# Optimization experiments

Measured on AMD Instinct MI355X. Metric: run time of the kernel, lower is better.

## Reference

```python
import jax, jax.numpy as jnp
import numpy as np


def _gcn_conv(x, edge_index, W, b):
    # PyG GCNConv: linear transform, add self-loops, symmetric deg^{-1/2} norm,
    # scatter-add aggregation from source (row) into target (col), then bias.
    N = x.shape[0]
    h = x @ W  # [N, out]
    loops = jnp.arange(N, dtype=edge_index.dtype)
    row = jnp.concatenate([edge_index[0], loops])  # sources j
    col = jnp.concatenate([edge_index[1], loops])  # targets i
    deg = jax.ops.segment_sum(jnp.ones_like(col, dtype=h.dtype), col, num_segments=N)
    dinv = jnp.where(deg > 0, jax.lax.rsqrt(deg), 0.0)
    norm = dinv[row] * dinv[col]  # [E+N]
    msgs = norm[:, None] * h[row]  # gather + scale
    out = jax.ops.segment_sum(msgs, col, num_segments=N)  # scatter-add
    return out + b


def setup_inputs() -> dict:
    key = jax.random.key(0)
    k1, k2, k3, k4 = jax.random.split(key, 4)
    N, E, F, H = 100000, 3200000, 128, 64
    x = jax.random.normal(k1, (N, F), dtype=jnp.float32)
    edge_index = jax.random.randint(k2, (2, E), 0, N, dtype=jnp.int64)
    W1 = jax.random.normal(k3, (F, H), dtype=jnp.float32) * (1.0 / np.sqrt(F))
    b1 = jnp.zeros((H,), dtype=jnp.float32)
    W2 = jax.random.normal(k4, (H, 1), dtype=jnp.float32) * (1.0 / np.sqrt(H))
    b2 = jnp.zeros((1,), dtype=jnp.float32)
    return {"x": x, "edge_index": edge_index, "W1": W1, "b1": b1, "W2": W2, "b2": b2}


def reference(x, edge_index, W1, b1, W2, b2):
    # eval mode: dropout is identity
    h = _gcn_conv(x, edge_index, W1, b1)
    h = jax.nn.relu(h)
    h = _gcn_conv(h, edge_index, W2, b2)  # [N, 1]
    return jnp.mean(h, axis=0)  # [1]
```

## Files before the change

kernel.cpp:

```cpp
#include <hip/hip_runtime.h>
#include <hip/hip_bf16.h>
#include <stdint.h>


#define F_IN 128
#define H_DIM 64
#define BKT_SH 7
#define BKT_SZ 128
#define MAXBKT 1024
#define PWG 256
#define PTHR 256
#define FINBLK 2048

typedef int   i4 __attribute__((ext_vector_type(4)));
typedef float f4 __attribute__((ext_vector_type(4)));
typedef float fv2 __attribute__((ext_vector_type(2)));

#if defined(__has_builtin)
#if __has_builtin(__builtin_amdgcn_cvt_pk_f32_fp8) && __has_builtin(__builtin_amdgcn_cvt_pk_fp8_f32)
#define HW_FP8 1
#endif
#endif

__device__ __forceinline__ float sw_dec_e4m3(unsigned b) {
    unsigned s = b & 0x80, e = (b >> 3) & 15, mm = b & 7;
    float v;
    if (e) v = __uint_as_float(((e + 120u) << 23) | (mm << 20));
    else   v = (float)mm * 0.001953125f;
    return s ? -v : v;
}
__device__ __forceinline__ unsigned sw_enc_e4m3(float f) {
    unsigned s = (__float_as_uint(f) & 0x80000000u) ? 0x80u : 0u;
    float a = fminf(fabsf(f), 448.0f);
    if (a < 9.765625e-4f) return s;
    if (a < 0.015625f) {
        int k = (int)rintf(a * 512.0f);
        if (k > 7) return s | 0x08;
        return s | (unsigned)k;
    }
    int e; float mant = frexpf(a, &e);
    int q = (int)rintf((mant * 2.0f - 1.0f) * 8.0f);
    int E = e - 1;
    if (q == 8) { q = 0; E += 1; }
    if (E > 8) { E = 8; q = 6; }
    return s | ((unsigned)(E + 7) << 3) | (unsigned)q;
}

__device__ __forceinline__ float2 f8pair(unsigned u) {
#ifdef HW_FP8
    fv2 r = __builtin_amdgcn_cvt_pk_f32_fp8((int)u, false);
    return make_float2(r.x, r.y);
#else
    return make_float2(sw_dec_e4m3(u & 0xff), sw_dec_e4m3((u >> 8) & 0xff));
#endif
}
__device__ __forceinline__ unsigned f8pack4(float v0, float v1, float v2, float v3) {
#ifdef HW_FP8
    unsigned pk = (unsigned)__builtin_amdgcn_cvt_pk_fp8_f32(v0, v1, 0, false);
    pk = (unsigned)__builtin_amdgcn_cvt_pk_fp8_f32(v2, v3, (int)pk, true);
    return pk;
#else
    return sw_enc_e4m3(v0) | (sw_enc_e4m3(v1) << 8) |
           (sw_enc_e4m3(v2) << 16) | (sw_enc_e4m3(v3) << 24);
#endif
}

__global__ __launch_bounds__(PTHR) void k_hist1(const int* __restrict__ col,
                                                int* __restrict__ histG,
                                                int E, int nbkt, int chunk) {
    __shared__ int h[MAXBKT];
    for (int i = threadIdx.x; i < nbkt; i += PTHR) h[i] = 0;
    __syncthreads();
    int s = blockIdx.x * chunk, e = min(E, s + chunk);
    if (s < e) {
        int s4 = s >> 2, e4 = e >> 2;
        const i4* c4 = (const i4*)col;
        int t = s4 + threadIdx.x;
        for (; t + 3 * PTHR < e4; t += 4 * PTHR) {
            i4 a = __builtin_nontemporal_load(c4 + t);
            i4 b = __builtin_nontemporal_load(c4 + t + PTHR);
            i4 c = __builtin_nontemporal_load(c4 + t + 2 * PTHR);
            i4 d = __builtin_nontemporal_load(c4 + t + 3 * PTHR);
            atomicAdd(&h[a.x >> BKT_SH], 1); atomicAdd(&h[a.y >> BKT_SH], 1);
            atomicAdd(&h[a.z >> BKT_SH], 1); atomicAdd(&h[a.w >> BKT_SH], 1);
            atomicAdd(&h[b.x >> BKT_SH], 1); atomicAdd(&h[b.y >> BKT_SH], 1);
            atomicAdd(&h[b.z >> BKT_SH], 1); atomicAdd(&h[b.w >> BKT_SH], 1);
            atomicAdd(&h[c.x >> BKT_SH], 1); atomicAdd(&h[c.y >> BKT_SH], 1);
            atomicAdd(&h[c.z >> BKT_SH], 1); atomicAdd(&h[c.w >> BKT_SH], 1);
            atomicAdd(&h[d.x >> BKT_SH], 1); atomicAdd(&h[d.y >> BKT_SH], 1);
            atomicAdd(&h[d.z >> BKT_SH], 1); atomicAdd(&h[d.w >> BKT_SH], 1);
        }
        for (; t < e4; t += PTHR) {
            i4 a = __builtin_nontemporal_load(c4 + t);
            atomicAdd(&h[a.x >> BKT_SH], 1); atomicAdd(&h[a.y >> BKT_SH], 1);
            atomicAdd(&h[a.z >> BKT_SH], 1); atomicAdd(&h[a.w >> BKT_SH], 1);
        }
        for (int i = (e4 << 2) + threadIdx.x; i < e; i += PTHR)
            atomicAdd(&h[col[i] >> BKT_SH], 1);
    }
    __syncthreads();
    for (int i = threadIdx.x; i < nbkt; i += PTHR)
        histG[(size_t)i * PWG + blockIdx.x] = h[i];
}

__global__ __launch_bounds__(PWG) void k_hscan_a(int* __restrict__ histG,
                                                 int* __restrict__ total, int nbkt) {
    __shared__ int s[PWG];
    int b = blockIdx.x, t = threadIdx.x;
    int v = histG[(size_t)b * PWG + t];
    s[t] = v;
    __syncthreads();
    for (int d = 1; d < PWG; d <<= 1) {
        int a = (t >= d) ? s[t - d] : 0;
        __syncthreads();
        s[t] += a;
        __syncthreads();
    }
    histG[(size_t)b * PWG + t] = s[t] - v;
    if (t == PWG - 1) total[b] = s[t];
}

__global__ __launch_bounds__(1024) void k_hscan_b(const int* __restrict__ total,
                                                  int* __restrict__ bstart, int nbkt) {
    __shared__ int s[1024];
    int t = threadIdx.x;
    int v = (t < nbkt) ? total[t] : 0;
    s[t] = v;
    __syncthreads();
    for (int d = 1; d < 1024; d <<= 1) {
        int a = (t >= d) ? s[t - d] : 0;
        __syncthreads();
        s[t] += a;
        __syncthreads();
    }
    if (t < nbkt) bstart[t] = s[t] - v;
    if (t == nbkt - 1) bstart[nbkt] = s[t];
}

__global__ __launch_bounds__(PTHR) void k_part(const int* __restrict__ row,
                                               const int* __restrict__ col,
                                               const int* __restrict__ histG,
                                               const int* __restrict__ bstart,
                                               unsigned int* __restrict__ part,
                                               int E, int nbkt, int chunk) {
    __shared__ int cur[MAXBKT];
    for (int i = threadIdx.x; i < nbkt; i += PTHR)
        cur[i] = bstart[i] + histG[(size_t)i * PWG + blockIdx.x];
    __syncthreads();
    int s = blockIdx.x * chunk, e = min(E, s + chunk);
    if (s >= e) return;
    int s4 = s >> 2, e4 = e >> 2;
    const i4* c4 = (const i4*)col;
    const i4* r4 = (const i4*)row;
    int t = s4 + threadIdx.x;
    for (; t + PTHR < e4; t += 2 * PTHR) {
        i4 ca = __builtin_nontemporal_load(c4 + t);
        i4 ra = __builtin_nontemporal_load(r4 + t);
        i4 cb = __builtin_nontemporal_load(c4 + t + PTHR);
        i4 rb = __builtin_nontemporal_load(r4 + t + PTHR);
        int p;
        p = atomicAdd(&cur[ca.x >> BKT_SH], 1);
        part[p] = ((unsigned int)ra.x << BKT_SH) | (unsigned int)(ca.x & (BKT_SZ - 1));
        p = atomicAdd(&cur[ca.y >> BKT_SH], 1);
        part[p] = ((unsigned int)ra.y << BKT_SH) | (unsigned int)(ca.y & (BKT_SZ - 1));
        p = atomicAdd(&cur[ca.z >> BKT_SH], 1);
        part[p] = ((unsigned int)ra.z << BKT_SH) | (unsigned int)(ca.z & (BKT_SZ - 1));
        p = atomicAdd(&cur[ca.w >> BKT_SH], 1);
        part[p] = ((unsigned int)ra.w << BKT_SH) | (unsigned int)(ca.w & (BKT_SZ - 1));
        p = atomicAdd(&cur[cb.x >> BKT_SH], 1);
        part[p] = ((unsigned int)rb.x << BKT_SH) | (unsigned int)(cb.x & (BKT_SZ - 1));
        p = atomicAdd(&cur[cb.y >> BKT_SH], 1);
        part[p] = ((unsigned int)rb.y << BKT_SH) | (unsigned int)(cb.y & (BKT_SZ - 1));
        p = atomicAdd(&cur[cb.z >> BKT_SH], 1);
        part[p] = ((unsigned int)rb.z << BKT_SH) | (unsigned int)(cb.z & (BKT_SZ - 1));
        p = atomicAdd(&cur[cb.w >> BKT_SH], 1);
        part[p] = ((unsigned int)rb.w << BKT_SH) | (unsigned int)(cb.w & (BKT_SZ - 1));
    }
    for (; t < e4; t += PTHR) {
        i4 ca = __builtin_nontemporal_load(c4 + t);
        i4 ra = __builtin_nontemporal_load(r4 + t);
        int p;
        p = atomicAdd(&cur[ca.x >> BKT_SH], 1);
        part[p] = ((unsigned int)ra.x << BKT_SH) | (unsigned int)(ca.x & (BKT_SZ - 1));
        p = atomicAdd(&cur[ca.y >> BKT_SH], 1);
        part[p] = ((unsigned int)ra.y << BKT_SH) | (unsigned int)(ca.y & (BKT_SZ - 1));
        p = atomicAdd(&cur[ca.z >> BKT_SH], 1);
        part[p] = ((unsigned int)ra.z << BKT_SH) | (unsigned int)(ca.z & (BKT_SZ - 1));
        p = atomicAdd(&cur[ca.w >> BKT_SH], 1);
        part[p] = ((unsigned int)ra.w << BKT_SH) | (unsigned int)(ca.w & (BKT_SZ - 1));
    }
    for (int i = (e4 << 2) + threadIdx.x; i < e; i += PTHR) {
        int c = col[i], r = row[i];
        int p = atomicAdd(&cur[c >> BKT_SH], 1);
        part[p] = ((unsigned int)r << BKT_SH) | (unsigned int)(c & (BKT_SZ - 1));
    }
}

__global__ __launch_bounds__(PTHR) void k_csr(const unsigned int* __restrict__ part,
                                              const int* __restrict__ bstart,
                                              int* __restrict__ offs,
                                              float* __restrict__ dinv,
                                              int* __restrict__ csr,
                                              int N, int E, int nbkt) {
    __shared__ int dg[BKT_SZ];
    __shared__ int sc[BKT_SZ];
    __shared__ int cur[BKT_SZ];
    int b = blockIdx.x, tid = threadIdx.x;
    if (tid < BKT_SZ) dg[tid] = 0;
    __syncthreads();
    int s = bstart[b], e = bstart[b + 1];
    for (int i = s + tid; i < e; i += PTHR)
        atomicAdd(&dg[part[i] & (BKT_SZ - 1)], 1);
    __syncthreads();
    if (tid < BKT_SZ) sc[tid] = dg[tid];
    __syncthreads();
    for (int d = 1; d < BKT_SZ; d <<= 1) {
        int v = (tid < BKT_SZ && tid >= d) ? sc[tid - d] : 0;
        __syncthreads();
        if (tid < BKT_SZ) sc[tid] += v;
        __syncthreads();
    }
    if (tid < BKT_SZ) {
        int ex = sc[tid] - dg[tid];
        cur[tid] = ex;
        int g = b * BKT_SZ + tid;
        if (g < N) {
            offs[g] = s + ex;
            dinv[g] = rsqrtf((float)dg[tid] + 1.0f);
        }
    }
    if (b == 0 && tid == 0) offs[N] = E;
    __syncthreads();
    for (int i = s + tid; i < e; i += PTHR) {
        unsigned int u = part[i];
        int cl = u & (BKT_SZ - 1);
        int p = atomicAdd(&cur[cl], 1);
        csr[s + p] = u >> BKT_SH;
    }
}

__global__ __launch_bounds__(256) void k_gemm1(const float* __restrict__ x,
                                               const float* __restrict__ W1,
                                               const float* __restrict__ dinv,
                                               unsigned int* __restrict__ xw8,
                                               int N) {
    __shared__ float xs[64 * 132];
    __shared__ float ws[128 * 64];
    int tid = threadIdx.x;
    int row0 = blockIdx.x * 64;

    const float4* w4 = (const float4*)W1;
    float4* ws4 = (float4*)ws;
#pragma unroll
    for (int i = 0; i < 8; i++) ws4[tid + 256 * i] = w4[tid + 256 * i];

#pragma unroll
    for (int i = 0; i < 8; i++) {
        int idx = tid + 256 * i;
        int r = idx >> 5;
        int c = idx & 31;
        f4 v = {0.f, 0.f, 0.f, 0.f};
        int gr = row0 + r;
        if (gr < N) v = __builtin_nontemporal_load((const f4*)x + (size_t)gr * 32 + c);
        *(f4*)&xs[r * 132 + c * 4] = v;
    }
    __syncthreads();

    int tx = tid & 15, ty = tid >> 4;
    float acc[4][4] = {};
#pragma unroll 4
    for (int k = 0; k < 128; k++) {
        float4 wv = *(const float4*)&ws[k * 64 + tx * 4];
#pragma unroll
        for (int i = 0; i < 4; i++) {
            float xv = xs[(ty * 4 + i) * 132 + k];
            acc[i][0] += xv * wv.x;
            acc[i][1] += xv * wv.y;
            acc[i][2] += xv * wv.z;
            acc[i][3] += xv * wv.w;
        }
    }
#pragma unroll
    for (int i = 0; i < 4; i++) {
        int gr = row0 + ty * 4 + i;
        if (gr < N) {
            float dsc = dinv[gr];
            unsigned pk = f8pack4(acc[i][0] * dsc, acc[i][1] * dsc,
                                  acc[i][2] * dsc, acc[i][3] * dsc);
            xw8[(size_t)gr * 16 + tx] = pk;
        }
    }
}

__global__ __launch_bounds__(256) void k_agg(const ushort* __restrict__ xw8,
                                             const int* __restrict__ csr,
                                             const int* __restrict__ offs,
                                             const float* __restrict__ dinv,
                                             const float* __restrict__ b1,
                                             const float* __restrict__ W2,
                                             float* __restrict__ yp, int N) {
    int wid = (blockIdx.x * blockDim.x + threadIdx.x) >> 6;
    int lane = threadIdx.x & 63;
    if (wid >= N) return;
    int m = lane & 31, half = lane >> 5;

    float di = dinv[wid];
    float2 bv = ((const float2*)b1)[m];
    float2 wv = ((const float2*)W2)[m];

    float a0 = 0.f, a1 = 0.f;
    if (half == 0) {
        float2 sv = f8pair(xw8[(size_t)wid * 32 + m]);
        a0 += sv.x; a1 += sv.y;
    }
    int p = offs[wid], pe = offs[wid + 1];
    for (; p + 16 <= pe; p += 16) {
        int j0 = csr[p + 0 + half];
        int j1 = csr[p + 2 + half];
        int j2 = csr[p + 4 + half];
        int j3 = csr[p + 6 + half];
        int j4 = csr[p + 8 + half];
        int j5 = csr[p + 10 + half];
        int j6 = csr[p + 12 + half];
        int j7 = csr[p + 14 + half];
        ushort u0 = xw8[(size_t)j0 * 32 + m];
        ushort u1 = xw8[(size_t)j1 * 32 + m];
        ushort u2 = xw8[(size_t)j2 * 32 + m];
        ushort u3 = xw8[(size_t)j3 * 32 + m];
        ushort u4 = xw8[(size_t)j4 * 32 + m];
        ushort u5 = xw8[(size_t)j5 * 32 + m];
        ushort u6 = xw8[(size_t)j6 * 32 + m];
        ushort u7 = xw8[(size_t)j7 * 32 + m];
        float2 v0 = f8pair(u0), v1 = f8pair(u1), v2 = f8pair(u2), v3 = f8pair(u3);
        float2 v4 = f8pair(u4), v5 = f8pair(u5), v6 = f8pair(u6), v7 = f8pair(u7);
        a0 += ((v0.x + v1.x) + (v2.x + v3.x)) + ((v4.x + v5.x) + (v6.x + v7.x));
        a1 += ((v0.y + v1.y) + (v2.y + v3.y)) + ((v4.y + v5.y) + (v6.y + v7.y));
    }
    for (; p + 8 <= pe; p += 8) {
        int j0 = csr[p + 0 + half];
        int j1 = csr[p + 2 + half];
        int j2 = csr[p + 4 + half];
        int j3 = csr[p + 6 + half];
        float2 v0 = f8pair(xw8[(size_t)j0 * 32 + m]);
        float2 v1 = f8pair(xw8[(size_t)j1 * 32 + m]);
        float2 v2 = f8pair(xw8[(size_t)j2 * 32 + m]);
        float2 v3 = f8pair(xw8[(size_t)j3 * 32 + m]);
        a0 += (v0.x + v1.x) + (v2.x + v3.x);
        a1 += (v0.y + v1.y) + (v2.y + v3.y);
    }
    for (; p + 2 <= pe; p += 2) {
        int j = csr[p + half];
        float2 v = f8pair(xw8[(size_t)j * 32 + m]);
        a0 += v.x; a1 += v.y;
    }
    if (p < pe && half == 0) {
        int j = csr[p];
        float2 v = f8pair(xw8[(size_t)j * 32 + m]);
        a0 += v.x; a1 += v.y;
    }
    a0 += __shfl_xor(a0, 32, 64);
    a1 += __shfl_xor(a1, 32, 64);
    float h0 = fmaxf(bv.x + di * a0, 0.f);
    float h1 = fmaxf(bv.y + di * a1, 0.f);
    float v = h0 * wv.x + h1 * wv.y;
#pragma unroll
    for (int d = 16; d > 0; d >>= 1) v += __shfl_xor(v, d, 64);
    if (lane == 0) yp[wid] = di * v;
}

__global__ __launch_bounds__(256) void k_final2(const int* __restrict__ row,
                                                const int* __restrict__ col,
                                                const float* __restrict__ dinv,
                                                const float* __restrict__ yp,
                                                float* __restrict__ partial,
                                                int N, int E) {
    int tid = blockIdx.x * blockDim.x + threadIdx.x;
    int nthr = gridDim.x * blockDim.x;
    float local = 0.f;
    int E4 = E >> 2;
    const i4* r4 = (const i4*)row;
    const i4* c4 = (const i4*)col;
    for (int t = tid; t < E4; t += nthr) {
        i4 r = __builtin_nontemporal_load(r4 + t);
        i4 c = __builtin_nontemporal_load(c4 + t);
        local += yp[r.x] * dinv[c.x] + yp[r.y] * dinv[c.y]
               + yp[r.z] * dinv[c.z] + yp[r.w] * dinv[c.w];
    }
    for (int e = (E4 << 2) + tid; e < E; e += nthr)
        local += yp[row[e]] * dinv[col[e]];
    int N4 = N >> 2;
    for (int t = tid; t < N4; t += nthr) {
        f4 d = *((const f4*)dinv + t);
        f4 yv = *((const f4*)yp + t);
        local += d.x * yv.x + d.y * yv.y + d.z * yv.z + d.w * yv.w;
    }
    for (int i = (N4 << 2) + tid; i < N; i += nthr)
        local += dinv[i] * yp[i];
#pragma unroll
    for (int d = 32; d > 0; d >>= 1) local += __shfl_xor(local, d, 64);
    __shared__ float wsum[4];
    int lane = threadIdx.x & 63, w = threadIdx.x >> 6;
    if (lane == 0) wsum[w] = local;
    __syncthreads();
    if (threadIdx.x == 0)
        partial[blockIdx.x] = (wsum[0] + wsum[1]) + (wsum[2] + wsum[3]);
}

__global__ __launch_bounds__(256) void k_write(const float* __restrict__ partial,
                                               const float* __restrict__ b2,
                                               float* __restrict__ out, int nb, int N) {
    float s = 0.f;
    for (int i = threadIdx.x; i < nb; i += 256) s += partial[i];
#pragma unroll
    for (int d = 32; d > 0; d >>= 1) s += __shfl_xor(s, d, 64);
    __shared__ float wsum[4];
    int lane = threadIdx.x & 63, w = threadIdx.x >> 6;
    if (lane == 0) wsum[w] = s;
    __syncthreads();
    if (threadIdx.x == 0)
        out[0] = b2[0] + ((wsum[0] + wsum[1]) + (wsum[2] + wsum[3])) / (float)N;
}

extern "C" void kernel_launch(void* const* d_in, const int* in_sizes, int n_in,
                              void* d_out, int out_size, void* d_ws, size_t ws_size,
                              hipStream_t stream) {
    const float* x  = (const float*)d_in[0];
    const int*   ei = (const int*)d_in[1];
    const float* W1 = (const float*)d_in[2];
    const float* b1 = (const float*)d_in[3];
    const float* W2 = (const float*)d_in[4];
    const float* b2 = (const float*)d_in[5];

    int N = in_sizes[0] / F_IN;
    int E = in_sizes[1] / 2;
    const int* erow = ei;
    const int* ecol = ei + E;

    int NBKT = (N + BKT_SZ - 1) >> BKT_SH;
    int chunk = (((E + PWG - 1) / PWG) + 3) & ~3;

    char* w = (char*)d_ws;
    auto take = [&](size_t bytes) {
        char* p = w;
        w += (bytes + 255) & ~(size_t)255;
        return p;
    };
    int*          histG   = (int*)take((size_t)NBKT * PWG * 4);
    int*          total   = (int*)take((size_t)NBKT * 4);
    int*          bstart  = (int*)take((size_t)(NBKT + 1) * 4);
    unsigned int* part    = (unsigned int*)take((size_t)E * 4);
    int*          csr     = (int*)take((size_t)E * 4);
    int*          offs    = (int*)take((size_t)(N + 1) * 4);
    float*        dinv    = (float*)take((size_t)N * 4);
    float*        yp      = (float*)take((size_t)N * 4);
    float*        partial = (float*)take((size_t)FINBLK * 4);
    unsigned int* xw8     = (unsigned int*)take((size_t)N * H_DIM);
    (void)ws_size;

    float* out = (float*)d_out;

    k_hist1<<<PWG, PTHR, 0, stream>>>(ecol, histG, E, NBKT, chunk);
    k_hscan_a<<<NBKT, PWG, 0, stream>>>(histG, total, NBKT);
    k_hscan_b<<<1, 1024, 0, stream>>>(total, bstart, NBKT);
    k_part<<<PWG, PTHR, 0, stream>>>(erow, ecol, histG, bstart, part, E, NBKT, chunk);
    k_csr<<<NBKT, PTHR, 0, stream>>>(part, bstart, offs, dinv, csr, N, E, NBKT);
    k_gemm1<<<(N + 63) / 64, 256, 0, stream>>>(x, W1, dinv, xw8, N);
    k_agg<<<((size_t)N * 64 + 255) / 256, 256, 0, stream>>>((const ushort*)xw8, csr, offs, dinv, b1, W2, yp, N);
    k_final2<<<FINBLK, 256, 0, stream>>>(erow, ecol, dinv, yp, partial, N, E);
    k_write<<<1, 256, 0, stream>>>(partial, b2, out, FINBLK, N);
}
```

Measured before the change: 215.1 us.

## Tile-local partitioning with coalesced scatter, LDS-staged CSR build, CSR-based final reduction

The partition kernel now processes edges in 4096-edge tiles. Each tile is grouped by bucket in LDS with a local histogram and scan, then written to global memory in contiguous runs instead of as per-edge random scattered stores. Buckets widen to 256 nodes (fewer buckets). The CSR build stages each bucket in LDS before writing it out coalesced, falling back to direct writes for large buckets. The second-layer reduction now walks the CSR per target node instead of rereading the raw row and col arrays, adding extra syncs and LDS pressure in exchange for fewer scattered global writes and reads.

Measured after the change: 195.6 us. 9.1% less time.

```diff
diff --git a/kernel.cpp b/kernel.cpp
--- a/kernel.cpp
+++ b/kernel.cpp
@@ -5,11 +5,14 @@
 
 #define F_IN 128
 #define H_DIM 64
-#define BKT_SH 7
-#define BKT_SZ 128
-#define MAXBKT 1024
+#define BKT_SH 8
+#define BKT_SZ 256
+#define MAXBKT 512
 #define PWG 256
 #define PTHR 256
+#define PPTHR 512
+#define TILE 4096
+#define CSR_CAP 10240
 #define FINBLK 2048
 
 typedef int   i4 __attribute__((ext_vector_type(4)));
@@ -81,22 +84,22 @@
             i4 b = __builtin_nontemporal_load(c4 + t + PTHR);
             i4 c = __builtin_nontemporal_load(c4 + t + 2 * PTHR);
             i4 d = __builtin_nontemporal_load(c4 + t + 3 * PTHR);
-            atomicAdd(&h[a.x >> BKT_SH], 1); atomicAdd(&h[a.y >> BKT_SH], 1);
-            atomicAdd(&h[a.z >> BKT_SH], 1); atomicAdd(&h[a.w >> BKT_SH], 1);
-            atomicAdd(&h[b.x >> BKT_SH], 1); atomicAdd(&h[b.y >> BKT_SH], 1);
-            atomicAdd(&h[b.z >> BKT_SH], 1); atomicAdd(&h[b.w >> BKT_SH], 1);
-            atomicAdd(&h[c.x >> BKT_SH], 1); atomicAdd(&h[c.y >> BKT_SH], 1);
-            atomicAdd(&h[c.z >> BKT_SH], 1); atomicAdd(&h[c.w >> BKT_SH], 1);
-            atomicAdd(&h[d.x >> BKT_SH], 1); atomicAdd(&h[d.y >> BKT_SH], 1);
-            atomicAdd(&h[d.z >> BKT_SH], 1); atomicAdd(&h[d.w >> BKT_SH], 1);
+            atomicAdd(&h[(unsigned)a.x >> BKT_SH], 1); atomicAdd(&h[(unsigned)a.y >> BKT_SH], 1);
+            atomicAdd(&h[(unsigned)a.z >> BKT_SH], 1); atomicAdd(&h[(unsigned)a.w >> BKT_SH], 1);
+            atomicAdd(&h[(unsigned)b.x >> BKT_SH], 1); atomicAdd(&h[(unsigned)b.y >> BKT_SH], 1);
+            atomicAdd(&h[(unsigned)b.z >> BKT_SH], 1); atomicAdd(&h[(unsigned)b.w >> BKT_SH], 1);
+            atomicAdd(&h[(unsigned)c.x >> BKT_SH], 1); atomicAdd(&h[(unsigned)c.y >> BKT_SH], 1);
+            atomicAdd(&h[(unsigned)c.z >> BKT_SH], 1); atomicAdd(&h[(unsigned)c.w >> BKT_SH], 1);
+            atomicAdd(&h[(unsigned)d.x >> BKT_SH], 1); atomicAdd(&h[(unsigned)d.y >> BKT_SH], 1);
+            atomicAdd(&h[(unsigned)d.z >> BKT_SH], 1); atomicAdd(&h[(unsigned)d.w >> BKT_SH], 1);
         }
         for (; t < e4; t += PTHR) {
             i4 a = __builtin_nontemporal_load(c4 + t);
-            atomicAdd(&h[a.x >> BKT_SH], 1); atomicAdd(&h[a.y >> BKT_SH], 1);
-            atomicAdd(&h[a.z >> BKT_SH], 1); atomicAdd(&h[a.w >> BKT_SH], 1);
+            atomicAdd(&h[(unsigned)a.x >> BKT_SH], 1); atomicAdd(&h[(unsigned)a.y >> BKT_SH], 1);
+            atomicAdd(&h[(unsigned)a.z >> BKT_SH], 1); atomicAdd(&h[(unsigned)a.w >> BKT_SH], 1);
         }
         for (int i = (e4 << 2) + threadIdx.x; i < e; i += PTHR)
-            atomicAdd(&h[col[i] >> BKT_SH], 1);
+            atomicAdd(&h[(unsigned)col[i] >> BKT_SH], 1);
     }
     __syncthreads();
     for (int i = threadIdx.x; i < nbkt; i += PTHR)
@@ -137,62 +140,53 @@
     if (t == nbkt - 1) bstart[nbkt] = s[t];
 }
 
-__global__ __launch_bounds__(PTHR) void k_part(const int* __restrict__ row,
-                                               const int* __restrict__ col,
-                                               const int* __restrict__ histG,
-                                               const int* __restrict__ bstart,
-                                               unsigned int* __restrict__ part,
-                                               int E, int nbkt, int chunk) {
-    __shared__ int cur[MAXBKT];
-    for (int i = threadIdx.x; i < nbkt; i += PTHR)
-        cur[i] = bstart[i] + histG[(size_t)i * PWG + blockIdx.x];
-    __syncthreads();
-    int s = blockIdx.x * chunk, e = min(E, s + chunk);
-    if (s >= e) return;
-    int s4 = s >> 2, e4 = e >> 2;
-    const i4* c4 = (const i4*)col;
-    const i4* r4 = (const i4*)row;
-    int t = s4 + threadIdx.x;
-    for (; t + PTHR < e4; t += 2 * PTHR) {
-        i4 ca = __builtin_nontemporal_load(c4 + t);
-        i4 ra = __builtin_nontemporal_load(r4 + t);
-        i4 cb = __builtin_nontemporal_load(c4 + t + PTHR);
-        i4 rb = __builtin_nontemporal_load(r4 + t + PTHR);
-        int p;
-        p = atomicAdd(&cur[ca.x >> BKT_SH], 1);
-        part[p] = ((unsigned int)ra.x << BKT_SH) | (unsigned int)(ca.x & (BKT_SZ - 1));
-        p = atomicAdd(&cur[ca.y >> BKT_SH], 1);
-        part[p] = ((unsigned int)ra.y << BKT_SH) | (unsigned int)(ca.y & (BKT_SZ - 1));
-        p = atomicAdd(&cur[ca.z >> BKT_SH], 1);
-        part[p] = ((unsigned int)ra.z << BKT_SH) | (unsigned int)(ca.z & (BKT_SZ - 1));
-        p = atomicAdd(&cur[ca.w >> BKT_SH], 1);
-        part[p] = ((unsigned int)ra.w << BKT_SH) | (unsigned int)(ca.w & (BKT_SZ - 1));
-        p = atomicAdd(&cur[cb.x >> BKT_SH], 1);
-        part[p] = ((unsigned int)rb.x << BKT_SH) | (unsigned int)(cb.x & (BKT_SZ - 1));
-        p = atomicAdd(&cur[cb.y >> BKT_SH], 1);
-        part[p] = ((unsigned int)rb.y << BKT_SH) | (unsigned int)(cb.y & (BKT_SZ - 1));
-        p = atomicAdd(&cur[cb.z >> BKT_SH], 1);
-        part[p] = ((unsigned int)rb.z << BKT_SH) | (unsigned int)(cb.z & (BKT_SZ - 1));
-        p = atomicAdd(&cur[cb.w >> BKT_SH], 1);
-        part[p] = ((unsigned int)rb.w << BKT_SH) | (unsigned int)(cb.w & (BKT_SZ - 1));
-    }
-    for (; t < e4; t += PTHR) {
-        i4 ca = __builtin_nontemporal_load(c4 + t);
-        i4 ra = __builtin_nontemporal_load(r4 + t);
-        int p;
-        p = atomicAdd(&cur[ca.x >> BKT_SH], 1);
-        part[p] = ((unsigned int)ra.x << BKT_SH) | (unsigned int)(ca.x & (BKT_SZ - 1));
-        p = atomicAdd(&cur[ca.y >> BKT_SH], 1);
-        part[p] = ((unsigned int)ra.y << BKT_SH) | (unsigned int)(ca.y & (BKT_SZ - 1));
-        p = atomicAdd(&cur[ca.z >> BKT_SH], 1);
-        part[p] = ((unsigned int)ra.z << BKT_SH) | (unsigned int)(ca.z & (BKT_SZ - 1));
-        p = atomicAdd(&cur[ca.w >> BKT_SH], 1);
-        part[p] = ((unsigned int)ra.w << BKT_SH) | (unsigned int)(ca.w & (BKT_SZ - 1));
-    }
-    for (int i = (e4 << 2) + threadIdx.x; i < e; i += PTHR) {
-        int c = col[i], r = row[i];
-        int p = atomicAdd(&cur[c >> BKT_SH], 1);
-        part[p] = ((unsigned int)r << BKT_SH) | (unsigned int)(c & (BKT_SZ - 1));
+__global__ __launch_bounds__(PPTHR) void k_part(const int* __restrict__ row,
+                                                const int* __restrict__ col,
+                                                const int* __restrict__ histG,
+                                                const int* __restrict__ bstart,
+                                                unsigned int* __restrict__ part,
+                                                int E, int nbkt, int chunk) {
+    __shared__ int hist[MAXBKT], hbase[MAXBKT], curl[MAXBKT], gcur[MAXBKT];
+    __shared__ int ssc[PPTHR];
+    __shared__ unsigned grouped[TILE];
+    __shared__ ushort bkt16[TILE];
+    int tid = threadIdx.x, wg = blockIdx.x;
+    for (int i = tid; i < nbkt; i += PPTHR)
+        gcur[i] = bstart[i] + histG[(size_t)i * PWG + wg];
+    int s = wg * chunk, e = min(E, s + chunk);
+    for (int ts = s; ts < e; ts += TILE) {
+        int te = min(e, ts + TILE), tc = te - ts;
+        for (int i = tid; i < nbkt; i += PPTHR) hist[i] = 0;
+        __syncthreads();
+        for (int i = ts + tid; i < te; i += PPTHR)
+            atomicAdd(&hist[(unsigned)col[i] >> BKT_SH], 1);
+        __syncthreads();
+        int v = (tid < nbkt) ? hist[tid] : 0;
+        ssc[tid] = v;
+        __syncthreads();
+        for (int d = 1; d < PPTHR; d <<= 1) {
+            int a = (tid >= d) ? ssc[tid - d] : 0;
+            __syncthreads();
+            ssc[tid] += a;
+            __syncthreads();
+        }
+        if (tid < nbkt) { hbase[tid] = ssc[tid] - v; curl[tid] = ssc[tid] - v; }
+        __syncthreads();
+        for (int i = ts + tid; i < te; i += PPTHR) {
+            int c = col[i], r = row[i];
+            int b = (unsigned)c >> BKT_SH;
+            int p = atomicAdd(&curl[b], 1);
+            grouped[p] = ((unsigned)r << BKT_SH) | (unsigned)(c & (BKT_SZ - 1));
+            bkt16[p] = (ushort)b;
+        }
+        __syncthreads();
+        for (int q = tid; q < tc; q += PPTHR) {
+            int b = bkt16[q];
+            part[gcur[b] + (q - hbase[b])] = grouped[q];
+        }
+        __syncthreads();
+        for (int i = tid; i < nbkt; i += PPTHR) gcur[i] += hist[i];
+        __syncthreads();
     }
 }
 
@@ -202,40 +196,48 @@
                                               float* __restrict__ dinv,
                                               int* __restrict__ csr,
                                               int N, int E, int nbkt) {
-    __shared__ int dg[BKT_SZ];
-    __shared__ int sc[BKT_SZ];
-    __shared__ int cur[BKT_SZ];
+    __shared__ int dg[BKT_SZ], sc[BKT_SZ], cur[BKT_SZ];
+    __shared__ int stage[CSR_CAP];
     int b = blockIdx.x, tid = threadIdx.x;
-    if (tid < BKT_SZ) dg[tid] = 0;
-    __syncthreads();
-    int s = bstart[b], e = bstart[b + 1];
+    dg[tid] = 0;
+    __syncthreads();
+    int s = bstart[b], e = bstart[b + 1], cnt = e - s;
     for (int i = s + tid; i < e; i += PTHR)
         atomicAdd(&dg[part[i] & (BKT_SZ - 1)], 1);
     __syncthreads();
-    if (tid < BKT_SZ) sc[tid] = dg[tid];
+    int v = dg[tid];
+    sc[tid] = v;
     __syncthreads();
     for (int d = 1; d < BKT_SZ; d <<= 1) {
-        int v = (tid < BKT_SZ && tid >= d) ? sc[tid - d] : 0;
-        __syncthreads();
-        if (tid < BKT_SZ) sc[tid] += v;
-        __syncthreads();
-    }
-    if (tid < BKT_SZ) {
-        int ex = sc[tid] - dg[tid];
-        cur[tid] = ex;
-        int g = b * BKT_SZ + tid;
-        if (g < N) {
-            offs[g] = s + ex;
-            dinv[g] = rsqrtf((float)dg[tid] + 1.0f);
-        }
+        int a = (tid >= d) ? sc[tid - d] : 0;
+        __syncthreads();
+        sc[tid] += a;
+        __syncthreads();
+    }
+    int ex = sc[tid] - v;
+    cur[tid] = ex;
+    int g = b * BKT_SZ + tid;
+    if (g < N) {
+        offs[g] = s + ex;
+        dinv[g] = rsqrtf((float)v + 1.0f);
     }
     if (b == 0 && tid == 0) offs[N] = E;
     __syncthreads();
-    for (int i = s + tid; i < e; i += PTHR) {
-        unsigned int u = part[i];
-        int cl = u & (BKT_SZ - 1);
-        int p = atomicAdd(&cur[cl], 1);
-        csr[s + p] = u >> BKT_SH;
+    if (cnt <= CSR_CAP) {
+        for (int i = s + tid; i < e; i += PTHR) {
+            unsigned u = part[i];
+            int p = atomicAdd(&cur[u & (BKT_SZ - 1)], 1);
+            stage[p] = (int)(u >> BKT_SH);
+        }
+        __syncthreads();
+        for (int q = tid; q < cnt; q += PTHR)
+            csr[s + q] = stage[q];
+    } else {
+        for (int i = s + tid; i < e; i += PTHR) {
+            unsigned u = part[i];
+            int p = atomicAdd(&cur[u & (BKT_SZ - 1)], 1);
+            csr[s + p] = (int)(u >> BKT_SH);
+        }
     }
 }
 
@@ -368,39 +370,26 @@
     if (lane == 0) yp[wid] = di * v;
 }
 
-__global__ __launch_bounds__(256) void k_final2(const int* __restrict__ row,
-                                                const int* __restrict__ col,
+__global__ __launch_bounds__(256) void k_final2(const int* __restrict__ csr,
+                                                const int* __restrict__ offs,
                                                 const float* __restrict__ dinv,
                                                 const float* __restrict__ yp,
-                                                float* __restrict__ partial,
-                                                int N, int E) {
-    int tid = blockIdx.x * blockDim.x + threadIdx.x;
-    int nthr = gridDim.x * blockDim.x;
-    float local = 0.f;
-    int E4 = E >> 2;
-    const i4* r4 = (const i4*)row;
-    const i4* c4 = (const i4*)col;
-    for (int t = tid; t < E4; t += nthr) {
-        i4 r = __builtin_nontemporal_load(r4 + t);
-        i4 c = __builtin_nontemporal_load(c4 + t);
-        local += yp[r.x] * dinv[c.x] + yp[r.y] * dinv[c.y]
-               + yp[r.z] * dinv[c.z] + yp[r.w] * dinv[c.w];
-    }
-    for (int e = (E4 << 2) + tid; e < E; e += nthr)
-        local += yp[row[e]] * dinv[col[e]];
-    int N4 = N >> 2;
-    for (int t = tid; t < N4; t += nthr) {
-        f4 d = *((const f4*)dinv + t);
-        f4 yv = *((const f4*)yp + t);
-        local += d.x * yv.x + d.y * yv.y + d.z * yv.z + d.w * yv.w;
-    }
-    for (int i = (N4 << 2) + tid; i < N; i += nthr)
-        local += dinv[i] * yp[i];
-#pragma unroll
-    for (int d = 32; d > 0; d >>= 1) local += __shfl_xor(local, d, 64);
+                                                float* __restrict__ partial, int N) {
+    int lane = threadIdx.x & 63, w = threadIdx.x >> 6;
+    int nwave_tot = gridDim.x * 4;
+    int wid0 = blockIdx.x * 4 + w;
+    float wpart = 0.f;
+    for (int i = wid0; i < N; i += nwave_tot) {
+        int p0 = offs[i], p1 = offs[i + 1];
+        float s = (lane == 0) ? yp[i] : 0.f;
+        for (int p = p0 + lane; p < p1; p += 64)
+            s += yp[csr[p]];
+#pragma unroll
+        for (int d = 32; d > 0; d >>= 1) s += __shfl_xor(s, d, 64);
+        if (lane == 0) wpart += dinv[i] * s;
+    }
     __shared__ float wsum[4];
-    int lane = threadIdx.x & 63, w = threadIdx.x >> 6;
-    if (lane == 0) wsum[w] = local;
+    if (lane == 0) wsum[w] = wpart;
     __syncthreads();
     if (threadIdx.x == 0)
         partial[blockIdx.x] = (wsum[0] + wsum[1]) + (wsum[2] + wsum[3]);
@@ -462,10 +451,10 @@
     k_hist1<<<PWG, PTHR, 0, stream>>>(ecol, histG, E, NBKT, chunk);
     k_hscan_a<<<NBKT, PWG, 0, stream>>>(histG, total, NBKT);
     k_hscan_b<<<1, 1024, 0, stream>>>(total, bstart, NBKT);
-    k_part<<<PWG, PTHR, 0, stream>>>(erow, ecol, histG, bstart, part, E, NBKT, chunk);
+    k_part<<<PWG, PPTHR, 0, stream>>>(erow, ecol, histG, bstart, part, E, NBKT, chunk);
     k_csr<<<NBKT, PTHR, 0, stream>>>(part, bstart, offs, dinv, csr, N, E, NBKT);
     k_gemm1<<<(N + 63) / 64, 256, 0, stream>>>(x, W1, dinv, xw8, N);
     k_agg<<<((size_t)N * 64 + 255) / 256, 256, 0, stream>>>((const ushort*)xw8, csr, offs, dinv, b1, W2, yp, N);
-    k_final2<<<FINBLK, 256, 0, stream>>>(erow, ecol, dinv, yp, partial, N, E);
+    k_final2<<<FINBLK, 256, 0, stream>>>(csr, offs, dinv, yp, partial, N);
     k_write<<<1, 256, 0, stream>>>(partial, b2, out, FINBLK, N);
 }
```
